# Optimization experiments

Measured on AMD Instinct MI355X. Metric: run time of the kernel, lower is better.

## Reference

```python
import jax, jax.numpy as jnp
import numpy as np

B, S, E, H = 4, 4096, 1024, 128

def setup_inputs() -> dict:
    key = jax.random.key(0)
    kx, kk, kq, kv = jax.random.split(key, 4)
    x = jax.random.normal(kx, (B, S, E), dtype=jnp.float32)
    # torch nn.Linear weights are [out_features, in_features]
    Wk = jax.random.normal(kk, (H, E), dtype=jnp.float32) * (E ** -0.5)
    Wq = jax.random.normal(kq, (H, E), dtype=jnp.float32) * (E ** -0.5)
    Wv = jax.random.normal(kv, (H, E), dtype=jnp.float32) * (E ** -0.5)
    return {"x": x, "Wk": Wk, "Wq": Wq, "Wv": Wv}

def reference(x, Wk, Wq, Wv):
    # projections: y = x @ W.T  (bias-free nn.Linear)
    k = jnp.einsum('bse,he->bsh', x, Wk)
    q = jnp.einsum('bse,he->bsh', x, Wq)
    v = jnp.einsum('bse,he->bsh', x, Wv)
    emb = x.shape[-1]
    # scores scaled by embedding_size**-0.5 (as in the source, not head_size)
    scores = jnp.einsum('bqh,bkh->bqk', q, k) * (emb ** -0.5)  # [B,S,S]
    # causal mask: positions j > i get -inf
    i = jnp.arange(scores.shape[-2])[:, None]
    j = jnp.arange(scores.shape[-1])[None, :]
    scores = jnp.where(j > i, jnp.float32(-jnp.inf), scores)
    probs = jax.nn.softmax(scores, axis=-1)
    # dropout is identity in eval mode
    out = jnp.einsum('bqk,bkh->bqh', probs, v)  # [B,S,H]
    return out
```

## Files before the change

### kernel.cpp

```cpp
#include <hip/hip_runtime.h>

typedef short bf16x8 __attribute__((ext_vector_type(8)));
typedef float f32x4 __attribute__((ext_vector_type(4)));

#define MFMA16(a, b, c) __builtin_amdgcn_mfma_f32_16x16x32_bf16(a, b, c, 0, 0, 0)

constexpr int Bn = 4, Sn = 4096, En = 1024, Hn = 128;

__device__ inline unsigned short f2bf(float f) {
    unsigned int u = __builtin_bit_cast(unsigned int, f);
    u += 0x7fff + ((u >> 16) & 1);
    return (unsigned short)(u >> 16);
}

__device__ inline unsigned int pk2(float a, float b) {
    unsigned int ua = __builtin_bit_cast(unsigned int, a) + 0x8000u;
    unsigned int ub = __builtin_bit_cast(unsigned int, b) + 0x8000u;
    return __builtin_amdgcn_perm(ub, ua, 0x07060302u);
}

__global__ __launch_bounds__(256, 2) void proj_kernel(
    const float* __restrict__ x,
    const float* __restrict__ Wk, const float* __restrict__ Wq, const float* __restrict__ Wv,
    unsigned short* __restrict__ qb, unsigned short* __restrict__ kb,
    unsigned short* __restrict__ vbT)
{
    __shared__ unsigned short xs[64][68];
    __shared__ unsigned short wsm[128][68];

    const int gy = blockIdx.y;
    const float* W = (gy == 0) ? Wq : (gy == 1) ? Wk : Wv;

    const int m0 = blockIdx.x * 64;
    const int tid = threadIdx.x;
    const int lane = tid & 63, wave = tid >> 6;
    const int l15 = lane & 15, quad = lane >> 4;
    const int wm = (wave & 1) * 32;
    const int wn = (wave >> 1) * 64;

    f32x4 acc[2][4] = {};

    float4 xp[4], wp[8];
    for (int p = 0; p < 4; ++p) {
        int i = p * 256 + tid, row = i >> 4, c = (i & 15) * 4;
        xp[p] = *(const float4*)&x[(size_t)(m0 + row) * En + c];
    }
    for (int p = 0; p < 8; ++p) {
        int i = p * 256 + tid, row = i >> 4, c = (i & 15) * 4;
        wp[p] = *(const float4*)&W[(size_t)row * En + c];
    }

    for (int kc = 0; kc < En / 64; ++kc) {
        for (int p = 0; p < 4; ++p) {
            int i = p * 256 + tid, row = i >> 4, c = (i & 15) * 4;
            uint2 w2 = { pk2(xp[p].x, xp[p].y), pk2(xp[p].z, xp[p].w) };
            *(uint2*)&xs[row][c] = w2;
        }
        for (int p = 0; p < 8; ++p) {
            int i = p * 256 + tid, row = i >> 4, c = (i & 15) * 4;
            uint2 w2 = { pk2(wp[p].x, wp[p].y), pk2(wp[p].z, wp[p].w) };
            *(uint2*)&wsm[row][c] = w2;
        }
        __syncthreads();
        if (kc + 1 < En / 64) {
            int k0 = (kc + 1) * 64;
            for (int p = 0; p < 4; ++p) {
                int i = p * 256 + tid, row = i >> 4, c = (i & 15) * 4;
                xp[p] = *(const float4*)&x[(size_t)(m0 + row) * En + k0 + c];
            }
            for (int p = 0; p < 8; ++p) {
                int i = p * 256 + tid, row = i >> 4, c = (i & 15) * 4;
                wp[p] = *(const float4*)&W[(size_t)row * En + k0 + c];
            }
        }
        if (gy != 2) {
            for (int kk = 0; kk < 2; ++kk) {
                bf16x8 af[2], bfr[4];
                for (int i = 0; i < 2; ++i) af[i]  = *(const bf16x8*)&xs[wm + i * 16 + l15][kk * 32 + quad * 8];
                for (int j = 0; j < 4; ++j) bfr[j] = *(const bf16x8*)&wsm[wn + j * 16 + l15][kk * 32 + quad * 8];
                for (int i = 0; i < 2; ++i)
                    for (int j = 0; j < 4; ++j)
                        acc[i][j] = MFMA16(af[i], bfr[j], acc[i][j]);
            }
        } else {
            for (int kk = 0; kk < 2; ++kk) {
                bf16x8 aw[4], bx[2];
                for (int j = 0; j < 4; ++j) aw[j] = *(const bf16x8*)&wsm[wn + j * 16 + l15][kk * 32 + quad * 8];
                for (int i = 0; i < 2; ++i) bx[i] = *(const bf16x8*)&xs[wm + i * 16 + l15][kk * 32 + quad * 8];
                for (int i = 0; i < 2; ++i)
                    for (int j = 0; j < 4; ++j)
                        acc[i][j] = MFMA16(aw[j], bx[i], acc[i][j]);
            }
        }
        __syncthreads();
    }

    if (gy != 2) {
        unsigned short* ob = (gy == 0) ? qb : kb;
        for (int i = 0; i < 2; ++i) {
            int rowb = m0 + wm + i * 16 + quad * 4;
            for (int j = 0; j < 4; ++j) {
                int col = wn + j * 16 + l15;
                for (int r = 0; r < 4; ++r)
                    ob[(size_t)(rowb + r) * Hn + col] = f2bf(acc[i][j][r]);
            }
        }
    } else {
        for (int j = 0; j < 4; ++j) {
            int hb = wn + j * 16 + quad * 4;
            for (int i = 0; i < 2; ++i) {
                int sp = m0 + wm + i * 16 + l15;
                int bb = sp >> 12, ss = sp & 4095;
                for (int r = 0; r < 4; ++r)
                    vbT[((size_t)(bb * 128 + hb + r)) * Sn + ss] = f2bf(acc[i][j][r]);
            }
        }
    }
}

__global__ __launch_bounds__(256, 2) void attn_kernel(
    const unsigned short* __restrict__ qb, const unsigned short* __restrict__ kb,
    const unsigned short* __restrict__ vbT, float* __restrict__ out)
{
    __shared__ unsigned short ks[2][64][132];
    __shared__ unsigned short vt[2][128][68];
    __shared__ unsigned short ps[2][32][68];

    const int b = blockIdx.y;
    const int qt = (int)gridDim.x - 1 - (int)blockIdx.x;
    const int q0 = qt * 32;
    const int tid = threadIdx.x;
    const int lane = tid & 63, wave = tid >> 6;
    const int l15 = lane & 15, quad = lane >> 4;
    const int g = wave & 1;
    const int p = wave >> 1;
    const int tpp = tid & 127;

    const unsigned short* qg = qb + (size_t)(b * Sn + q0) * Hn;
    bf16x8 qf[4];
    {
        int qrow = g * 16 + l15;
        for (int f = 0; f < 4; ++f)
            qf[f] = *(const bf16x8*)&qg[qrow * Hn + f * 32 + quad * 8];
    }

    f32x4 o[8] = {};
    float m_r = -INFINITY, l_r = 0.f;

    const float cscale = 1.44269504089f * 0.03125f;
    const int nkt = q0 / 64 + 1;
    const int ni = (nkt + 1) >> 1;

    const unsigned short* kg = kb + (size_t)b * Sn * Hn;
    const unsigned short* vg = vbT + (size_t)b * 128 * Sn;

    bf16x8 kreg[8], vreg[8];
    {
        int kt0 = p * 64;
        for (int p8 = 0; p8 < 8; ++p8) {
            int i = p8 * 128 + tpp;
            kreg[p8] = *(const bf16x8*)&kg[(size_t)(kt0 + (i >> 4)) * Hn + (i & 15) * 8];
            vreg[p8] = *(const bf16x8*)&vg[(size_t)(i >> 3) * Sn + kt0 + (i & 7) * 8];
        }
    }

    for (int it = 0; it < ni; ++it) {
        const int kt = 2 * it + p;
        const bool active = kt < nkt;
        for (int p8 = 0; p8 < 8; ++p8) {
            int i = p8 * 128 + tpp;
            *(bf16x8*)&ks[p][i >> 4][(i & 15) * 8] = kreg[p8];
            *(bf16x8*)&vt[p][i >> 3][(i & 7) * 8] = vreg[p8];
        }
        __syncthreads();
        if (kt + 2 < nkt) {
            int kt0n = (kt + 2) * 64;
            for (int p8 = 0; p8 < 8; ++p8) {
                int i = p8 * 128 + tpp;
                kreg[p8] = *(const bf16x8*)&kg[(size_t)(kt0n + (i >> 4)) * Hn + (i & 15) * 8];
                vreg[p8] = *(const bf16x8*)&vg[(size_t)(i >> 3) * Sn + kt0n + (i & 7) * 8];
            }
        }
        if (active) {
            float u[4][4];
            for (int nt = 0; nt < 4; ++nt) {
                f32x4 s = {};
                for (int kk = 0; kk < 4; ++kk) {
                    bf16x8 kf = *(const bf16x8*)&ks[p][nt * 16 + l15][kk * 32 + quad * 8];
                    s = MFMA16(kf, qf[kk], s);
                }
                for (int r = 0; r < 4; ++r) u[nt][r] = s[r] * cscale;
            }
            if (kt == nkt - 1) {
                int kt0 = kt * 64;
                int qq = q0 + g * 16 + l15;
                for (int nt = 0; nt < 4; ++nt)
                    for (int r = 0; r < 4; ++r)
                        if (kt0 + nt * 16 + quad * 4 + r > qq) u[nt][r] = -INFINITY;
            }
            float mx = -INFINITY;
            for (int nt = 0; nt < 4; ++nt)
                for (int r = 0; r < 4; ++r) mx = fmaxf(mx, u[nt][r]);
            mx = fmaxf(mx, __shfl_xor(mx, 16));
            mx = fmaxf(mx, __shfl_xor(mx, 32));
            float mn = fmaxf(m_r, mx);
            float alpha = exp2f(m_r - mn);
            m_r = mn;
            float sum = 0.f;
            for (int nt = 0; nt < 4; ++nt)
                for (int r = 0; r < 4; ++r) {
                    float pv = exp2f(u[nt][r] - mn);
                    u[nt][r] = pv;
                    sum += pv;
                }
            sum += __shfl_xor(sum, 16);
            sum += __shfl_xor(sum, 32);
            l_r = l_r * alpha + sum;

            for (int nt = 0; nt < 4; ++nt) {
                uint2 w2 = { pk2(u[nt][0], u[nt][1]), pk2(u[nt][2], u[nt][3]) };
                *(uint2*)&ps[p][g * 16 + l15][nt * 16 + quad * 4] = w2;
            }
            for (int t = 0; t < 8; ++t) o[t] *= alpha;

            for (int k2 = 0; k2 < 2; ++k2) {
                bf16x8 pf = *(const bf16x8*)&ps[p][g * 16 + l15][k2 * 32 + quad * 8];
                for (int t = 0; t < 8; ++t) {
                    bf16x8 vf = *(const bf16x8*)&vt[p][t * 16 + l15][k2 * 32 + quad * 8];
                    o[t] = MFMA16(vf, pf, o[t]);
                }
            }
        }
        __syncthreads();
    }

    float* mo = (float*)&ks[0][0][0];
    float* ml = (float*)&vt[0][0][0];
    if (p == 1) {
        for (int t = 0; t < 8; ++t)
            for (int r = 0; r < 4; ++r)
                mo[(size_t)(g * 128 + t * 16 + quad * 4 + r) * 17 + l15] = o[t][r];
        if (quad == 0) {
            ml[g * 32 + l15] = m_r;
            ml[g * 32 + 16 + l15] = l_r;
        }
    }
    __syncthreads();
    if (p == 0) {
        float m1 = ml[g * 32 + l15];
        float l1 = ml[g * 32 + 16 + l15];
        float M = fmaxf(m_r, m1);
        float w0 = exp2f(m_r - M);
        float w1 = exp2f(m1 - M);
        float L = w0 * l_r + w1 * l1;
        float inv = 1.0f / L;
        float* og = out + (size_t)(b * Sn + q0 + g * 16 + l15) * Hn;
        for (int t = 0; t < 8; ++t) {
            float4 st;
            float* mor = &mo[(size_t)(g * 128 + t * 16 + quad * 4) * 17 + l15];
            st.x = (w0 * o[t][0] + w1 * mor[0 * 17]) * inv;
            st.y = (w0 * o[t][1] + w1 * mor[1 * 17]) * inv;
            st.z = (w0 * o[t][2] + w1 * mor[2 * 17]) * inv;
            st.w = (w0 * o[t][3] + w1 * mor[3 * 17]) * inv;
            *(float4*)&og[t * 16 + quad * 4] = st;
        }
    }
}

extern "C" void kernel_launch(void* const* d_in, const int* in_sizes, int n_in,
                              void* d_out, int out_size, void* d_ws, size_t ws_size,
                              hipStream_t stream)
{
    const float* x  = (const float*)d_in[0];
    const float* Wk = (const float*)d_in[1];
    const float* Wq = (const float*)d_in[2];
    const float* Wv = (const float*)d_in[3];
    float* out = (float*)d_out;

    unsigned short* qbuf  = (unsigned short*)d_ws;
    unsigned short* kbuf  = qbuf + (size_t)Bn * Sn * Hn;
    unsigned short* vbufT = kbuf + (size_t)Bn * Sn * Hn;

    proj_kernel<<<dim3(Bn * Sn / 64, 3), 256, 0, stream>>>(x, Wk, Wq, Wv, qbuf, kbuf, vbufT);
    attn_kernel<<<dim3(Sn / 32, Bn), 256, 0, stream>>>(qbuf, kbuf, vbufT, out);
}
```

Before: 209.0 us.

## Fuse Q/K/V projections into one pass with prepacked bf16 weights

```diff
diff --git a/kernel.cpp b/kernel.cpp
--- a/kernel.cpp
+++ b/kernel.cpp
@@ -19,101 +19,102 @@
     return __builtin_amdgcn_perm(ub, ua, 0x07060302u);
 }
 
+__global__ __launch_bounds__(256) void prep_kernel(
+    const float* __restrict__ Wk, const float* __restrict__ Wq, const float* __restrict__ Wv,
+    unsigned short* __restrict__ wb)
+{
+    int gy = blockIdx.x >> 5;
+    const float* src = (gy == 0) ? Wq : (gy == 1) ? Wk : Wv;
+    unsigned short* dst = wb + (size_t)gy * Hn * En;
+    int t = (blockIdx.x & 31) * 256 + threadIdx.x;
+    const float4* s4 = (const float4*)src;
+    for (int i = 0; i < 4; ++i) {
+        float4 v = s4[(size_t)t * 4 + i];
+        uint2 w2 = { pk2(v.x, v.y), pk2(v.z, v.w) };
+        *(uint2*)&dst[(size_t)t * 16 + i * 4] = w2;
+    }
+}
+
 __global__ __launch_bounds__(256, 2) void proj_kernel(
-    const float* __restrict__ x,
-    const float* __restrict__ Wk, const float* __restrict__ Wq, const float* __restrict__ Wv,
+    const float* __restrict__ x, const unsigned short* __restrict__ wb,
     unsigned short* __restrict__ qb, unsigned short* __restrict__ kb,
     unsigned short* __restrict__ vbT)
 {
-    __shared__ unsigned short xs[64][68];
-    __shared__ unsigned short wsm[128][68];
-
-    const int gy = blockIdx.y;
-    const float* W = (gy == 0) ? Wq : (gy == 1) ? Wk : Wv;
-
-    const int m0 = blockIdx.x * 64;
+    __shared__ unsigned short xs[2][32][68];
+
+    const int m0 = blockIdx.x * 32;
     const int tid = threadIdx.x;
     const int lane = tid & 63, wave = tid >> 6;
     const int l15 = lane & 15, quad = lane >> 4;
-    const int wm = (wave & 1) * 32;
-    const int wn = (wave >> 1) * 64;
-
-    f32x4 acc[2][4] = {};
-
-    float4 xp[4], wp[8];
-    for (int p = 0; p < 4; ++p) {
-        int i = p * 256 + tid, row = i >> 4, c = (i & 15) * 4;
-        xp[p] = *(const float4*)&x[(size_t)(m0 + row) * En + c];
-    }
-    for (int p = 0; p < 8; ++p) {
-        int i = p * 256 + tid, row = i >> 4, c = (i & 15) * 4;
-        wp[p] = *(const float4*)&W[(size_t)row * En + c];
-    }
+    const int wn = wave * 32;
+
+    f32x4 acc[3][2][2] = {};
+
+    float4 xp[2];
+    for (int p = 0; p < 2; ++p) {
+        int i = p * 256 + tid, row = i >> 4, c4 = (i & 15) * 4;
+        xp[p] = *(const float4*)&x[(size_t)(m0 + row) * En + c4];
+    }
+
+    const unsigned short* wrow = wb + (size_t)(wn + l15) * En + quad * 8;
 
     for (int kc = 0; kc < En / 64; ++kc) {
-        for (int p = 0; p < 4; ++p) {
-            int i = p * 256 + tid, row = i >> 4, c = (i & 15) * 4;
+        const int c = kc & 1;
+        const int k0 = kc * 64;
+
+        bf16x8 wf[3][2][2];
+        for (int gy = 0; gy < 3; ++gy)
+            for (int j = 0; j < 2; ++j)
+                for (int kk = 0; kk < 2; ++kk)
+                    wf[gy][j][kk] = *(const bf16x8*)&wrow[(size_t)gy * Hn * En + (size_t)j * 16 * En + k0 + kk * 32];
+
+        for (int p = 0; p < 2; ++p) {
+            int i = p * 256 + tid, row = i >> 4, cc = (i & 15) * 4;
             uint2 w2 = { pk2(xp[p].x, xp[p].y), pk2(xp[p].z, xp[p].w) };
-            *(uint2*)&xs[row][c] = w2;
-        }
-        for (int p = 0; p < 8; ++p) {
-            int i = p * 256 + tid, row = i >> 4, c = (i & 15) * 4;
-            uint2 w2 = { pk2(wp[p].x, wp[p].y), pk2(wp[p].z, wp[p].w) };
-            *(uint2*)&wsm[row][c] = w2;
+            *(uint2*)&xs[c][row][cc] = w2;
         }
         __syncthreads();
-        if (kc + 1 < En / 64) {
-            int k0 = (kc + 1) * 64;
-            for (int p = 0; p < 4; ++p) {
-                int i = p * 256 + tid, row = i >> 4, c = (i & 15) * 4;
-                xp[p] = *(const float4*)&x[(size_t)(m0 + row) * En + k0 + c];
-            }
-            for (int p = 0; p < 8; ++p) {
-                int i = p * 256 + tid, row = i >> 4, c = (i & 15) * 4;
-                wp[p] = *(const float4*)&W[(size_t)row * En + k0 + c];
-            }
-        }
-        if (gy != 2) {
-            for (int kk = 0; kk < 2; ++kk) {
-                bf16x8 af[2], bfr[4];
-                for (int i = 0; i < 2; ++i) af[i]  = *(const bf16x8*)&xs[wm + i * 16 + l15][kk * 32 + quad * 8];
-                for (int j = 0; j < 4; ++j) bfr[j] = *(const bf16x8*)&wsm[wn + j * 16 + l15][kk * 32 + quad * 8];
-                for (int i = 0; i < 2; ++i)
-                    for (int j = 0; j < 4; ++j)
-                        acc[i][j] = MFMA16(af[i], bfr[j], acc[i][j]);
-            }
-        } else {
-            for (int kk = 0; kk < 2; ++kk) {
-                bf16x8 aw[4], bx[2];
-                for (int j = 0; j < 4; ++j) aw[j] = *(const bf16x8*)&wsm[wn + j * 16 + l15][kk * 32 + quad * 8];
-                for (int i = 0; i < 2; ++i) bx[i] = *(const bf16x8*)&xs[wm + i * 16 + l15][kk * 32 + quad * 8];
-                for (int i = 0; i < 2; ++i)
-                    for (int j = 0; j < 4; ++j)
-                        acc[i][j] = MFMA16(aw[j], bx[i], acc[i][j]);
-            }
-        }
-        __syncthreads();
-    }
-
-    if (gy != 2) {
+
+        {
+            int kn = (kc + 1 < En / 64) ? kc + 1 : kc;
+            for (int p = 0; p < 2; ++p) {
+                int i = p * 256 + tid, row = i >> 4, c4 = (i & 15) * 4;
+                xp[p] = *(const float4*)&x[(size_t)(m0 + row) * En + kn * 64 + c4];
+            }
+        }
+
+        bf16x8 xf[2][2];
+        for (int i = 0; i < 2; ++i)
+            for (int kk = 0; kk < 2; ++kk)
+                xf[i][kk] = *(const bf16x8*)&xs[c][i * 16 + l15][kk * 32 + quad * 8];
+
+        for (int kk = 0; kk < 2; ++kk)
+            for (int i = 0; i < 2; ++i)
+                for (int j = 0; j < 2; ++j) {
+                    acc[0][i][j] = MFMA16(xf[i][kk], wf[0][j][kk], acc[0][i][j]);
+                    acc[1][i][j] = MFMA16(xf[i][kk], wf[1][j][kk], acc[1][i][j]);
+                    acc[2][i][j] = MFMA16(wf[2][j][kk], xf[i][kk], acc[2][i][j]);
+                }
+    }
+
+    for (int gy = 0; gy < 2; ++gy) {
         unsigned short* ob = (gy == 0) ? qb : kb;
         for (int i = 0; i < 2; ++i) {
-            int rowb = m0 + wm + i * 16 + quad * 4;
-            for (int j = 0; j < 4; ++j) {
+            int rowb = m0 + i * 16 + quad * 4;
+            for (int j = 0; j < 2; ++j) {
                 int col = wn + j * 16 + l15;
                 for (int r = 0; r < 4; ++r)
-                    ob[(size_t)(rowb + r) * Hn + col] = f2bf(acc[i][j][r]);
-            }
-        }
-    } else {
-        for (int j = 0; j < 4; ++j) {
-            int hb = wn + j * 16 + quad * 4;
-            for (int i = 0; i < 2; ++i) {
-                int sp = m0 + wm + i * 16 + l15;
-                int bb = sp >> 12, ss = sp & 4095;
-                for (int r = 0; r < 4; ++r)
-                    vbT[((size_t)(bb * 128 + hb + r)) * Sn + ss] = f2bf(acc[i][j][r]);
-            }
+                    ob[(size_t)(rowb + r) * Hn + col] = f2bf(acc[gy][i][j][r]);
+            }
+        }
+    }
+    for (int j = 0; j < 2; ++j) {
+        int hb = wn + j * 16 + quad * 4;
+        for (int i = 0; i < 2; ++i) {
+            int sp = m0 + i * 16 + l15;
+            int bb = sp >> 12, ss = sp & 4095;
+            for (int r = 0; r < 4; ++r)
+                vbT[((size_t)(bb * 128 + hb + r)) * Sn + ss] = f2bf(acc[2][i][j][r]);
         }
     }
 }
@@ -280,7 +281,9 @@
     unsigned short* qbuf  = (unsigned short*)d_ws;
     unsigned short* kbuf  = qbuf + (size_t)Bn * Sn * Hn;
     unsigned short* vbufT = kbuf + (size_t)Bn * Sn * Hn;
-
-    proj_kernel<<<dim3(Bn * Sn / 64, 3), 256, 0, stream>>>(x, Wk, Wq, Wv, qbuf, kbuf, vbufT);
+    unsigned short* wb    = vbufT + (size_t)Bn * Sn * Hn;
+
+    prep_kernel<<<96, 256, 0, stream>>>(Wk, Wq, Wv, wb);
+    proj_kernel<<<Bn * Sn / 32, 256, 0, stream>>>(x, wb, qbuf, kbuf, vbufT);
     attn_kernel<<<dim3(Sn / 32, Bn), 256, 0, stream>>>(qbuf, kbuf, vbufT, out);
 }
```

After: 227.4 us. +8.8%, slower.

## Stream K/V tiles straight into swizzled LDS with async loads, halve key tile

Applied to the files above, without the earlier changes.

```diff
diff --git a/kernel.cpp b/kernel.cpp
--- a/kernel.cpp
+++ b/kernel.cpp
@@ -6,6 +6,7 @@
 #define MFMA16(a, b, c) __builtin_amdgcn_mfma_f32_16x16x32_bf16(a, b, c, 0, 0, 0)
 
 constexpr int Bn = 4, Sn = 4096, En = 1024, Hn = 128;
+constexpr float CSCALE = 1.44269504089f * 0.03125f;
 
 __device__ inline unsigned short f2bf(float f) {
     unsigned int u = __builtin_bit_cast(unsigned int, f);
@@ -17,6 +18,11 @@
     unsigned int ua = __builtin_bit_cast(unsigned int, a) + 0x8000u;
     unsigned int ub = __builtin_bit_cast(unsigned int, b) + 0x8000u;
     return __builtin_amdgcn_perm(ub, ua, 0x07060302u);
+}
+
+__device__ inline void gld16(const unsigned short* g, unsigned short* l) {
+    __builtin_amdgcn_global_load_lds((const __attribute__((address_space(1))) void*)g,
+                                     (__attribute__((address_space(3))) void*)l, 16, 0, 0);
 }
 
 __global__ __launch_bounds__(256, 2) void proj_kernel(
@@ -97,12 +103,13 @@
 
     if (gy != 2) {
         unsigned short* ob = (gy == 0) ? qb : kb;
+        const float osc = (gy == 0) ? CSCALE : 1.0f;
         for (int i = 0; i < 2; ++i) {
             int rowb = m0 + wm + i * 16 + quad * 4;
             for (int j = 0; j < 4; ++j) {
                 int col = wn + j * 16 + l15;
                 for (int r = 0; r < 4; ++r)
-                    ob[(size_t)(rowb + r) * Hn + col] = f2bf(acc[i][j][r]);
+                    ob[(size_t)(rowb + r) * Hn + col] = f2bf(acc[i][j][r] * osc);
             }
         }
     } else {
@@ -122,9 +129,8 @@
     const unsigned short* __restrict__ qb, const unsigned short* __restrict__ kb,
     const unsigned short* __restrict__ vbT, float* __restrict__ out)
 {
-    __shared__ unsigned short ks[2][64][132];
-    __shared__ unsigned short vt[2][128][68];
-    __shared__ unsigned short ps[2][32][68];
+    __shared__ __align__(16) unsigned char smem[70144];
+    unsigned short* psb = (unsigned short*)(smem + 65536);
 
     const int b = blockIdx.y;
     const int qt = (int)gridDim.x - 1 - (int)blockIdx.x;
@@ -134,7 +140,6 @@
     const int l15 = lane & 15, quad = lane >> 4;
     const int g = wave & 1;
     const int p = wave >> 1;
-    const int tpp = tid & 127;
 
     const unsigned short* qg = qb + (size_t)(b * Sn + q0) * Hn;
     bf16x8 qf[4];
@@ -147,59 +152,57 @@
     f32x4 o[8] = {};
     float m_r = -INFINITY, l_r = 0.f;
 
-    const float cscale = 1.44269504089f * 0.03125f;
-    const int nkt = q0 / 64 + 1;
+    const int nkt = qt + 1;
     const int ni = (nkt + 1) >> 1;
 
     const unsigned short* kg = kb + (size_t)b * Sn * Hn;
     const unsigned short* vg = vbT + (size_t)b * 128 * Sn;
 
-    bf16x8 kreg[8], vreg[8];
-    {
-        int kt0 = p * 64;
-        for (int p8 = 0; p8 < 8; ++p8) {
-            int i = p8 * 128 + tpp;
-            kreg[p8] = *(const bf16x8*)&kg[(size_t)(kt0 + (i >> 4)) * Hn + (i & 15) * 8];
-            vreg[p8] = *(const bf16x8*)&vg[(size_t)(i >> 3) * Sn + kt0 + (i & 7) * 8];
-        }
-    }
+    unsigned short* psrow = &psb[(p * 32 + g * 16 + l15) * 36];
+
+    auto issue = [&](int kt, int c) {
+        char* base = (char*)smem + (p * 2 + c) * 16384;
+        int kt0 = kt * 32;
+        for (int j = 0; j < 4; ++j) {
+            int seg = (g * 4 + j) * 1024;
+            int dk = seg + lane * 16;
+            int key = dk >> 8, ch = (dk >> 4) & 15;
+            gld16(kg + (size_t)(kt0 + key) * Hn + ((ch ^ (key & 7)) << 3),
+                  (unsigned short*)(base + seg));
+            int h = dk >> 6, cc = (dk >> 4) & 3;
+            gld16(vg + (size_t)h * Sn + kt0 + ((cc ^ (h & 3)) << 3),
+                  (unsigned short*)(base + 8192 + seg));
+        }
+    };
+
+    if (p < nkt) issue(p, 0);
 
     for (int it = 0; it < ni; ++it) {
         const int kt = 2 * it + p;
-        const bool active = kt < nkt;
-        for (int p8 = 0; p8 < 8; ++p8) {
-            int i = p8 * 128 + tpp;
-            *(bf16x8*)&ks[p][i >> 4][(i & 15) * 8] = kreg[p8];
-            *(bf16x8*)&vt[p][i >> 3][(i & 7) * 8] = vreg[p8];
-        }
         __syncthreads();
-        if (kt + 2 < nkt) {
-            int kt0n = (kt + 2) * 64;
-            for (int p8 = 0; p8 < 8; ++p8) {
-                int i = p8 * 128 + tpp;
-                kreg[p8] = *(const bf16x8*)&kg[(size_t)(kt0n + (i >> 4)) * Hn + (i & 15) * 8];
-                vreg[p8] = *(const bf16x8*)&vg[(size_t)(i >> 3) * Sn + kt0n + (i & 7) * 8];
-            }
-        }
-        if (active) {
-            float u[4][4];
-            for (int nt = 0; nt < 4; ++nt) {
+        if (kt + 2 < nkt) issue(kt + 2, (it + 1) & 1);
+        if (kt < nkt) {
+            unsigned short* kbase = (unsigned short*)((char*)smem + (p * 2 + (it & 1)) * 16384);
+            unsigned short* vbase = kbase + 4096;
+
+            float u[2][4];
+            for (int nt = 0; nt < 2; ++nt) {
                 f32x4 s = {};
                 for (int kk = 0; kk < 4; ++kk) {
-                    bf16x8 kf = *(const bf16x8*)&ks[p][nt * 16 + l15][kk * 32 + quad * 8];
+                    int ch = (kk * 4 + quad) ^ (l15 & 7);
+                    bf16x8 kf = *(const bf16x8*)&kbase[(nt * 16 + l15) * 128 + ch * 8];
                     s = MFMA16(kf, qf[kk], s);
                 }
-                for (int r = 0; r < 4; ++r) u[nt][r] = s[r] * cscale;
+                for (int r = 0; r < 4; ++r) u[nt][r] = s[r];
             }
             if (kt == nkt - 1) {
-                int kt0 = kt * 64;
-                int qq = q0 + g * 16 + l15;
-                for (int nt = 0; nt < 4; ++nt)
+                int qq = g * 16 + l15;
+                for (int nt = 0; nt < 2; ++nt)
                     for (int r = 0; r < 4; ++r)
-                        if (kt0 + nt * 16 + quad * 4 + r > qq) u[nt][r] = -INFINITY;
+                        if (nt * 16 + quad * 4 + r > qq) u[nt][r] = -INFINITY;
             }
             float mx = -INFINITY;
-            for (int nt = 0; nt < 4; ++nt)
+            for (int nt = 0; nt < 2; ++nt)
                 for (int r = 0; r < 4; ++r) mx = fmaxf(mx, u[nt][r]);
             mx = fmaxf(mx, __shfl_xor(mx, 16));
             mx = fmaxf(mx, __shfl_xor(mx, 32));
@@ -207,7 +210,7 @@
             float alpha = exp2f(m_r - mn);
             m_r = mn;
             float sum = 0.f;
-            for (int nt = 0; nt < 4; ++nt)
+            for (int nt = 0; nt < 2; ++nt)
                 for (int r = 0; r < 4; ++r) {
                     float pv = exp2f(u[nt][r] - mn);
                     u[nt][r] = pv;
@@ -217,25 +220,24 @@
             sum += __shfl_xor(sum, 32);
             l_r = l_r * alpha + sum;
 
-            for (int nt = 0; nt < 4; ++nt) {
+            for (int nt = 0; nt < 2; ++nt) {
                 uint2 w2 = { pk2(u[nt][0], u[nt][1]), pk2(u[nt][2], u[nt][3]) };
-                *(uint2*)&ps[p][g * 16 + l15][nt * 16 + quad * 4] = w2;
+                *(uint2*)&psrow[nt * 16 + quad * 4] = w2;
             }
             for (int t = 0; t < 8; ++t) o[t] *= alpha;
 
-            for (int k2 = 0; k2 < 2; ++k2) {
-                bf16x8 pf = *(const bf16x8*)&ps[p][g * 16 + l15][k2 * 32 + quad * 8];
-                for (int t = 0; t < 8; ++t) {
-                    bf16x8 vf = *(const bf16x8*)&vt[p][t * 16 + l15][k2 * 32 + quad * 8];
-                    o[t] = MFMA16(vf, pf, o[t]);
-                }
-            }
-        }
-        __syncthreads();
-    }
-
-    float* mo = (float*)&ks[0][0][0];
-    float* ml = (float*)&vt[0][0][0];
+            bf16x8 pf = *(const bf16x8*)&psrow[quad * 8];
+            for (int t = 0; t < 8; ++t) {
+                int hh = t * 16 + l15;
+                bf16x8 vf = *(const bf16x8*)&vbase[hh * 32 + ((quad ^ (l15 & 3)) << 3)];
+                o[t] = MFMA16(vf, pf, o[t]);
+            }
+        }
+    }
+    __syncthreads();
+
+    float* mo = (float*)smem;
+    float* ml = (float*)(smem + 20480);
     if (p == 1) {
         for (int t = 0; t < 8; ++t)
             for (int r = 0; r < 4; ++r)
```

Result: slower. 213.5 us (+2.1%).
